# Performance work log

Measured on AMD Instinct MI355X. Metric: run time of the kernel, lower is better.

The kernel has to match this reference:

```python
import math
import jax, jax.numpy as jnp
import numpy as np

B, N, H, K = 8, 1024, 200, 3
EDGE_SIZE = 50

def _layernorm(x, g, b, eps=1e-20):
    mu = jnp.mean(x, -1, keepdims=True)
    var = jnp.mean((x - mu) ** 2, -1, keepdims=True)
    return (x - mu) / jnp.sqrt(var + eps) * g + b

def _bert_layer(x, mask_add, qw, qb, kw, kb, vw, vb, aow, aob, g1, b1, iw, ib, ow, ob, g2, b2):
    # single-head self-attention (num_heads=1 -> head_dim == H), eval mode (dropout = identity)
    q = x @ qw + qb
    k = x @ kw + kb
    v = x @ vw + vb
    scores = jnp.einsum('bnd,bmd->bnm', q, k) / math.sqrt(H) + mask_add  # [B,N,N]
    probs = jax.nn.softmax(scores, -1)
    ctx = jnp.einsum('bnm,bmd->bnd', probs, v)
    attn = _layernorm(ctx @ aow + aob + x, g1, b1)
    inter = jax.nn.gelu(attn @ iw + ib, approximate=False)
    return _layernorm(inter @ ow + ob + attn, g2, b2)

def setup_inputs():
    key = jax.random.key(0)
    ks = jax.random.split(key, 16)
    s = 0.02
    text = jax.random.normal(ks[0], (B, N, H), jnp.float32)
    adj1 = (jax.random.uniform(ks[1], (B, N, N)) < 0.02).astype(jnp.float32)
    adj1 = jnp.maximum(adj1, jnp.eye(N, dtype=jnp.float32))  # self loops
    adj2 = (jax.random.uniform(ks[2], (B, N, N)) < 0.02).astype(jnp.float32)
    edge1 = jax.random.randint(ks[3], (B, N, N), 0, EDGE_SIZE, jnp.int32)
    edge2 = jax.random.randint(ks[4], (B, N, N), 0, EDGE_SIZE, jnp.int32)
    lengths = jax.random.randint(ks[5], (B,), N // 2, N + 1)
    textmask = (jnp.arange(N)[None, :] < lengths[:, None]).astype(jnp.float32)
    def nrm(k, shape):
        return jax.random.normal(k, shape, jnp.float32) * s
    return dict(
        text=text, adj1=adj1, adj2=adj2, edge1=edge1, edge2=edge2, textmask=textmask,
        gcn_w=nrm(ks[6], (H, H)), mut_w=nrm(ks[7], (H, H)),
        qw=nrm(ks[8], (K, H, H)), qb=jnp.zeros((K, H), jnp.float32),
        kw=nrm(ks[9], (K, H, H)), kb=jnp.zeros((K, H), jnp.float32),
        vw=nrm(ks[10], (K, H, H)), vb=jnp.zeros((K, H), jnp.float32),
        aow=nrm(ks[11], (K, H, H)), aob=jnp.zeros((K, H), jnp.float32),
        ln1_g=jnp.ones((K, H), jnp.float32), ln1_b=jnp.zeros((K, H), jnp.float32),
        iw=nrm(ks[12], (K, H, H)), ib=jnp.zeros((K, H), jnp.float32),
        ow=nrm(ks[13], (K, H, H)), ob=jnp.zeros((K, H), jnp.float32),
        ln2_g=jnp.ones((K, H), jnp.float32), ln2_b=jnp.zeros((K, H), jnp.float32))

def reference(text, adj1, adj2, edge1, edge2, textmask, gcn_w, mut_w, qw, qb, kw, kb, vw, vb, aow, aob, ln1_g, ln1_b, iw, ib, ow, ob, ln2_g, ln2_b):
    # edge1/edge2 and edge_vocab are unused by the original forward
    adj = adj1 + adj2
    adj = jnp.where(adj >= 1.0, 1.0, adj)
    mask_add = ((1.0 - textmask) * -10000.0)[:, None, :]           # [B,1,N] key-side mask
    pair = textmask[:, :, None] * textmask[:, None, :]             # [B,N,N]
    pair_add = (1.0 - pair) * -10000.0
    denom = jnp.sum(adj, 2, keepdims=True) + 1e-07                 # [B,N,1]
    outs, output = text, text                                      # in_features == out_features path
    for i in range(K):
        outs = _bert_layer(outs, mask_add, qw[i], qb[i], kw[i], kb[i], vw[i], vb[i],
                           aow[i], aob[i], ln1_g[i], ln1_b[i], iw[i], ib[i], ow[i], ob[i], ln2_g[i], ln2_b[i])
        # GCN propagation: adj-matmul -> degree normalize -> relu -> residual (dropout = identity in eval)
        teout = output @ gcn_w
        output = jax.nn.relu(jnp.einsum('bnm,bmd->bnd', adj, teout) / denom) + output
        # selfalignment: dual masked softmax attention between outs and output
        logit = jnp.einsum('bnd,bmd->bnm', outs @ mut_w, output) + pair_add
        p_row = jax.nn.softmax(logit, -1)
        p_col = jax.nn.softmax(logit, -2)
        new_outs = jnp.einsum('bnm,bmd->bnd', p_row, output) * textmask[:, :, None] + outs
        output = jnp.einsum('bnm,bnd->bmd', p_col, outs) * textmask[:, :, None] + output
        outs = new_outs
    return outs, adj
```

## Files before the change

### kernel.cpp

```cpp
#include <hip/hip_runtime.h>
#include <hip/hip_bf16.h>
#include <math.h>

#define Bd 8
#define Nd 1024
#define Hd 200
#define HP 224
#define BN (Bd*Nd)
#define SZ_BNH ((size_t)BN*Hd)
#define SZ_BNN ((size_t)BN*Nd)
#define SZ_PAD ((size_t)BN*HP)

typedef __hip_bfloat16 bf16;
typedef __attribute__((ext_vector_type(8))) short bf16x8;
typedef __attribute__((ext_vector_type(4))) float f32x4;
typedef __attribute__((ext_vector_type(4))) short s16x4;

__device__ __forceinline__ float bf2f(bf16 v){ return __bfloat162float(v); }
__device__ __forceinline__ bf16 f2bf(float v){ return __float2bfloat16(v); }
__device__ __forceinline__ short bfb(float v){ bf16 h = f2bf(v); return *(short*)&h; }
__device__ __forceinline__ short lowb(float v){
  bf16 h = f2bf(v); bf16 l = f2bf(v - bf2f(h)); return *(short*)&l;
}

#define MFMA16(a,b,c) __builtin_amdgcn_mfma_f32_16x16x32_bf16((a),(b),(c),0,0,0)

__device__ __forceinline__ size_t tidx1024(int row, int k){
  return (size_t)(row>>4)*16384 + (size_t)((k>>5))*512
       + (size_t)(((k>>3)&3))*128 + (size_t)(row&15)*8 + (k&7);
}
__device__ __forceinline__ size_t tidxHP(int row, int k){
  return (size_t)(row>>4)*3584 + (size_t)((k>>5))*512
       + (size_t)(((k>>3)&3))*128 + (size_t)(row&15)*8 + (k&7);
}

__global__ void k_prep_masks(const float* __restrict__ tm, float* __restrict__ maskf,
                             float* __restrict__ maskadd){
  int i = blockIdx.x*256 + threadIdx.x;
  if (i < BN){ float m = tm[i]; maskf[i] = m; maskadd[i] = (1.f - m) * -10000.f; }
}

__global__ void k_prep_adj(const float* __restrict__ a1, const float* __restrict__ a2,
                           float* __restrict__ adj_out, float* __restrict__ denom){
  int r = blockIdx.x;
  const size_t base = (size_t)r * Nd;
  int t = threadIdx.x;
  float s = 0.f;
  for (int m = t; m < Nd; m += 256){
    float a = a1[base+m] + a2[base+m];
    a = a >= 1.f ? 1.f : a;
    adj_out[base+m] = a;
    s += a;
  }
  __shared__ float red[256];
  red[t] = s; __syncthreads();
  for (int st = 128; st > 0; st >>= 1){ if (t < st) red[t] += red[t+st]; __syncthreads(); }
  if (t == 0) denom[r] = red[0] + 1e-07f;
}

__global__ void k_copy2(const float* __restrict__ x, float* __restrict__ o1,
                        float* __restrict__ o2){
  size_t i = (size_t)blockIdx.x*256 + threadIdx.x;
  if (i < SZ_BNH){ float v = x[i]; o1[i] = v; o2[i] = v; }
}

__global__ void c_pad_split(const float* __restrict__ X, bf16* __restrict__ Oh,
                            bf16* __restrict__ Ol){
  size_t o = (size_t)blockIdx.x*256 + threadIdx.x;
  if (o >= SZ_PAD) return;
  int oi = (int)o;
  int panel = oi / 3584;
  int rem   = oi % 3584;
  int kt  = rem >> 9;
  int kg  = (rem >> 7) & 3;
  int r16 = (rem >> 3) & 15;
  int ke  = rem & 7;
  int row = panel*16 + r16;
  int k   = kt*32 + kg*8 + ke;
  float v = (k < Hd) ? X[(size_t)row*Hd + k] : 0.f;
  bf16 h = f2bf(v);
  Oh[o] = h; Ol[o] = f2bf(v - bf2f(h));
}

__global__ void c_padT_split(const float* __restrict__ X, bf16* __restrict__ Oh,
                             bf16* __restrict__ Ol){
  __shared__ float t[32][33];
  int b = blockIdx.z, m0 = blockIdx.x*32, d0 = blockIdx.y*32;
  int tx = threadIdx.x, ty = threadIdx.y;
  for (int i = ty; i < 32; i += 8){
    int d = d0 + tx;
    t[i][tx] = (d < Hd) ? X[((size_t)b*Nd + m0+i)*Hd + d] : 0.f;
  }
  __syncthreads();
  for (int i = ty; i < 32; i += 8){
    int row = d0 + i, kk = m0 + tx;
    size_t idx = (size_t)b*229376 + tidx1024(row, kk);
    float v = t[tx][i];
    bf16 h = f2bf(v);
    Oh[idx] = h; Ol[idx] = f2bf(v - bf2f(h));
  }
}

__global__ void c_w_split_all(const float* __restrict__ g, const float* __restrict__ m,
                              const float* __restrict__ q, const float* __restrict__ k,
                              const float* __restrict__ v, const float* __restrict__ ao,
                              const float* __restrict__ iw, const float* __restrict__ ow,
                              bf16* __restrict__ Oh, bf16* __restrict__ Ol){
  int mi = blockIdx.y;
  const float* W;
  if (mi == 0) W = g;
  else if (mi == 1) W = m;
  else {
    int gi = (mi-2)/3, si = (mi-2)%3;
    const float* bs[6] = {q, k, v, ao, iw, ow};
    W = bs[gi] + (size_t)si*Hd*Hd;
  }
  int o = blockIdx.x*256 + threadIdx.x;
  if (o >= HP*HP) return;
  int panel = o / 3584;
  int rem   = o % 3584;
  int kt  = rem >> 9;
  int kg  = (rem >> 7) & 3;
  int r16 = (rem >> 3) & 15;
  int ke  = rem & 7;
  int n   = panel*16 + r16;
  int kk  = kt*32 + kg*8 + ke;
  float val = (n < Hd && kk < Hd) ? W[kk*Hd + n] : 0.f;
  bf16 h = f2bf(val);
  Oh[(size_t)mi*HP*HP + o] = h; Ol[(size_t)mi*HP*HP + o] = f2bf(val - bf2f(h));
}

__global__ void c_cvt1024_t(const float* __restrict__ X, bf16* __restrict__ O){
  int b = blockIdx.z, kg = blockIdx.x, rg = blockIdx.y;
  int r = threadIdx.x >> 5, kl = threadIdx.x & 31;
  int row = rg*8 + r, k = kg*32 + kl;
  float v = X[(size_t)b*1048576 + (size_t)row*1024 + k];
  O[(size_t)b*1048576 + tidx1024(row, k)] = f2bf(v);
}

__global__ __launch_bounds__(256)
void k_rowsoftmax0(const float* __restrict__ S, bf16* __restrict__ Ph){
  __shared__ float red[256];
  size_t bid = blockIdx.x;
  size_t r = ((bid & 7) << 10) + (bid >> 3);
  int t = threadIdx.x;
  const f32x4 v4 = *(const f32x4*)(S + r*Nd + t*4);
  float mx = fmaxf(fmaxf(v4[0], v4[1]), fmaxf(v4[2], v4[3]));
  red[t] = mx; __syncthreads();
  for (int s = 128; s > 0; s >>= 1){ if (t < s) red[t] = fmaxf(red[t], red[t+s]); __syncthreads(); }
  mx = red[0]; __syncthreads();
  float e0 = __expf(v4[0] - mx), e1 = __expf(v4[1] - mx);
  float e2 = __expf(v4[2] - mx), e3 = __expf(v4[3] - mx);
  red[t] = (e0 + e1) + (e2 + e3); __syncthreads();
  for (int s = 128; s > 0; s >>= 1){ if (t < s) red[t] += red[t+s]; __syncthreads(); }
  float inv = 1.f / red[0];
  size_t obase = ((r >> 10) << 20) + (size_t)(((int)(r & 1023)) >> 4)*16384
               + (size_t)((int)r & 15)*8;
  int i = t*4;
  size_t idx = obase + (size_t)(i>>5)*512 + (size_t)((i>>3)&3)*128 + (i&7);
  s16x4 hv = { bfb(e0*inv), bfb(e1*inv), bfb(e2*inv), bfb(e3*inv) };
  *(s16x4*)(Ph + idx) = hv;
}

__global__ __launch_bounds__(256)
void k_rowsm8(const float* __restrict__ S, bf16* __restrict__ Ph,
              bf16* __restrict__ Pl, const float* __restrict__ cmax,
              const float* __restrict__ csum, bf16* __restrict__ PcH,
              bf16* __restrict__ PcL){
  __shared__ float rows[8][1028];
  int bq = blockIdx.x & 7;
  int rg = blockIdx.x >> 3;
  int n0 = rg*8;
  int t = threadIdx.x;
  int r_loc = t >> 5, j = t & 31;
  size_t r = ((size_t)bq << 10) + n0 + r_loc;
  const float* src = S + r*Nd;
  f32x4 v[8];
  float mx = -3.4e38f;
  #pragma unroll
  for (int kk = 0; kk < 8; kk++){
    v[kk] = *(const f32x4*)(src + kk*128 + j*4);
    *(f32x4*)(&rows[r_loc][kk*128 + j*4]) = v[kk];
    mx = fmaxf(mx, fmaxf(fmaxf(v[kk][0], v[kk][1]), fmaxf(v[kk][2], v[kk][3])));
  }
  #pragma unroll
  for (int off = 16; off >= 1; off >>= 1) mx = fmaxf(mx, __shfl_xor(mx, off));
  float e[8][4];
  float sum = 0.f;
  #pragma unroll
  for (int kk = 0; kk < 8; kk++){
    #pragma unroll
    for (int q = 0; q < 4; q++){ e[kk][q] = __expf(v[kk][q] - mx); }
    sum += (e[kk][0] + e[kk][1]) + (e[kk][2] + e[kk][3]);
  }
  #pragma unroll
  for (int off = 16; off >= 1; off >>= 1) sum += __shfl_xor(sum, off);
  float inv = 1.f / sum;
  size_t obase = ((size_t)bq << 20) + (size_t)((n0 + r_loc) >> 4)*16384
               + (size_t)((n0 + r_loc) & 15)*8;
  #pragma unroll
  for (int kk = 0; kk < 8; kk++){
    int i = kk*128 + j*4;
    size_t idx = obase + (size_t)(i>>5)*512 + (size_t)((i>>3)&3)*128 + (i&7);
    float p0 = e[kk][0]*inv, p1 = e[kk][1]*inv, p2 = e[kk][2]*inv, p3 = e[kk][3]*inv;
    s16x4 hv = { bfb(p0), bfb(p1), bfb(p2), bfb(p3) };
    *(s16x4*)(Ph + idx) = hv;
    s16x4 lv = { lowb(p0), lowb(p1), lowb(p2), lowb(p3) };
    *(s16x4*)(Pl + idx) = lv;
  }
  __syncthreads();
  const f32x4 c4 = *(const f32x4*)(cmax + bq*Nd + t*4);
  const f32x4 s4 = *(const f32x4*)(csum + bq*Nd + t*4);
  size_t nb = (size_t)bq*1048576 + (size_t)(rg>>2)*512 + (size_t)(rg&3)*128;
  #pragma unroll
  for (int mi = 0; mi < 4; mi++){
    int m = t*4 + mi;
    float cm = c4[mi], ci = 1.f / s4[mi];
    bf16x8 hv, lv;
    #pragma unroll
    for (int rr = 0; rr < 8; rr++){
      float p = __expf(rows[rr][m] - cm) * ci;
      bf16 h = f2bf(p);
      hv[rr] = *(short*)&h;
      bf16 l = f2bf(p - bf2f(h));
      lv[rr] = *(short*)&l;
    }
    size_t idx = nb + (size_t)(m>>4)*16384 + (size_t)(m&15)*8;
    *(bf16x8*)(PcH + idx) = hv;
    *(bf16x8*)(PcL + idx) = lv;
  }
}

__global__ void k_colcomb(const float* __restrict__ cpm, const float* __restrict__ cps,
                          float* __restrict__ cmax, float* __restrict__ csum){
  int i = blockIdx.x*256 + threadIdx.x;
  float M = cpm[i], S = cps[i];
  #pragma unroll
  for (int y = 1; y < 8; y++){
    float m2 = cpm[(size_t)y*BN + i], s2 = cps[(size_t)y*BN + i];
    float Mn = fmaxf(M, m2);
    S = S*__expf(M - Mn) + s2*__expf(m2 - Mn);
    M = Mn;
  }
  cmax[i] = M; csum[i] = S;
}

__global__ void k_add_ln(const float* __restrict__ X, const float* __restrict__ R,
                         const float* __restrict__ g, const float* __restrict__ bb,
                         float* __restrict__ Y, bf16* __restrict__ Ph,
                         bf16* __restrict__ Pl){
  int r = blockIdx.x, t = threadIdx.x;
  __shared__ float red[256];
  bool act = t < Hd;
  float v = 0.f;
  if (act) v = X[(size_t)r*Hd + t] + R[(size_t)r*Hd + t];
  red[t] = act ? v : 0.f; __syncthreads();
  for (int s = 128; s > 0; s >>= 1){ if (t < s) red[t] += red[t+s]; __syncthreads(); }
  float mu = red[0] * (1.f/Hd); __syncthreads();
  float d = act ? (v - mu) : 0.f;
  red[t] = d*d; __syncthreads();
  for (int s = 128; s > 0; s >>= 1){ if (t < s) red[t] += red[t+s]; __syncthreads(); }
  float var = red[0] * (1.f/Hd);
  float o = 0.f;
  if (act){
    float rs = 1.f / sqrtf(var + 1e-20f);
    o = (v - mu) * rs * g[t] + bb[t];
    Y[(size_t)r*Hd + t] = o;
  }
  if (Ph && t < HP){
    bf16 h = f2bf(o);
    size_t idx = tidxHP(r, t);
    Ph[idx] = h; Pl[idx] = f2bf(o - bf2f(h));
  }
}

__global__ __launch_bounds__(256)
void k_qkv(const bf16* __restrict__ Ah, const bf16* __restrict__ Al,
           const bf16* __restrict__ Wh0, const bf16* __restrict__ Wl0,
           bf16* __restrict__ QH, bf16* __restrict__ QL,
           bf16* __restrict__ KH, bf16* __restrict__ KL,
           bf16* __restrict__ VH, bf16* __restrict__ VL,
           const float* __restrict__ qb, const float* __restrict__ kb,
           const float* __restrict__ vb)
{
  constexpr int KP = HP;
  constexpr int STEPS = KP/32;
  int slice = blockIdx.z;
  int wave = threadIdx.x >> 6, lane = threadIdx.x & 63;
  int r0 = (blockIdx.y*4 + wave)*16;
  int c0 = blockIdx.x*64;
  int lm = lane & 15, lq = lane >> 4;
  const size_t PST = (size_t)16*KP;
  const size_t aT = (size_t)(r0>>4)*PST + (size_t)lane*8;
  const size_t bT = (size_t)slice*3*HP*HP + (size_t)(c0>>4)*PST + (size_t)lane*8;

  f32x4 acc[4] = {};
  bf16x8 pah[2], pal[2], pbh[2][4], pbl[2][4];
  pah[0] = *(const bf16x8*)(Ah + aT);
  pal[0] = *(const bf16x8*)(Al + aT);
  #pragma unroll
  for (int j = 0; j < 4; j++){
    pbh[0][j] = *(const bf16x8*)(Wh0 + bT + (size_t)j*PST);
    pbl[0][j] = *(const bf16x8*)(Wl0 + bT + (size_t)j*PST);
  }
  #pragma unroll
  for (int ki = 0; ki < STEPS; ki++){
    const int cb = ki & 1, nb = cb ^ 1;
    if (ki + 1 < STEPS){
      const size_t kn = (size_t)(ki+1)*512;
      pah[nb] = *(const bf16x8*)(Ah + aT + kn);
      pal[nb] = *(const bf16x8*)(Al + aT + kn);
      #pragma unroll
      for (int j = 0; j < 4; j++){
        pbh[nb][j] = *(const bf16x8*)(Wh0 + bT + (size_t)j*PST + kn);
        pbl[nb][j] = *(const bf16x8*)(Wl0 + bT + (size_t)j*PST + kn);
      }
    }
    #pragma unroll
    for (int j = 0; j < 4; j++) acc[j] = MFMA16(pah[cb], pbh[cb][j], acc[j]);
    #pragma unroll
    for (int j = 0; j < 4; j++) acc[j] = MFMA16(pah[cb], pbl[cb][j], acc[j]);
    #pragma unroll
    for (int j = 0; j < 4; j++) acc[j] = MFMA16(pal[cb], pbh[cb][j], acc[j]);
  }

  const float* bias = (slice == 0) ? qb : (slice == 1) ? kb : vb;
  if (slice < 2){
    bf16* Oh = (slice == 0) ? QH : KH;
    bf16* Ol = (slice == 0) ? QL : KL;
    #pragma unroll
    for (int j = 0; j < 4; j++){
      int col = c0 + j*16 + lm;
      if (col >= HP) continue;
      #pragma unroll
      for (int r = 0; r < 4; r++){
        int row = r0 + lq*4 + r;
        float o = (col < Hd) ? acc[j][r] + bias[col] : 0.f;
        bf16 h = f2bf(o);
        size_t idx = tidxHP(row, col);
        Oh[idx] = h; Ol[idx] = f2bf(o - bf2f(h));
      }
    }
  } else {
    __shared__ float tl[64][65];
    #pragma unroll
    for (int j = 0; j < 4; j++)
      #pragma unroll
      for (int r = 0; r < 4; r++)
        tl[wave*16 + lq*4 + r][j*16 + lm] = acc[j][r];
    __syncthreads();
    int b2 = (int)((blockIdx.y*64) >> 10);
    int m0 = (int)((blockIdx.y*64) & 1023);
    #pragma unroll
    for (int e = threadIdx.x; e < 4096; e += 256){
      int pan = e >> 10, rem = e & 1023;
      int r16 = (rem >> 3) & 15;
      int d = c0 + pan*16 + r16;
      if (d >= HP) continue;
      int kg = (rem >> 7) & 3;
      int k_loc = (rem >> 9)*32 + kg*8 + (rem & 7);
      float val = 0.f;
      if (d < Hd) val = tl[k_loc][pan*16 + r16] + bias[d];
      bf16 h = f2bf(val);
      size_t idx = (size_t)b2*229376 + (size_t)(d>>4)*16384
                 + (size_t)((m0 + k_loc)>>5)*512 + (size_t)kg*128
                 + (size_t)r16*8 + (rem & 7);
      VH[idx] = h; VL[idx] = f2bf(val - bf2f(h));
    }
  }
}

template<int EPI, int TERMS, int RI, int KP>
__global__ __launch_bounds__(256)
void k_mfma3(const bf16* __restrict__ Ah, const bf16* __restrict__ Al,
             const bf16* __restrict__ Bh, const bf16* __restrict__ Bl,
             float* __restrict__ Y, bf16* __restrict__ Ybh, bf16* __restrict__ Ybl,
             const float* __restrict__ bias, const float* __restrict__ e0,
             const float* __restrict__ e1,
             size_t sAb, size_t sBb, float scale,
             float* __restrict__ cpm, float* __restrict__ cps)
{
  int b = blockIdx.z;
  int wave = threadIdx.x >> 6, lane = threadIdx.x & 63;
  int r0 = (blockIdx.y*4 + wave)*(RI*16);
  int c0 = blockIdx.x*64;
  int lm = lane & 15, lq = lane >> 4;
  const size_t PST = (size_t)16*KP;
  const size_t aT = (size_t)b*sAb + (size_t)(r0>>4)*PST + (size_t)lane*8;
  const size_t bT = (size_t)b*sBb + (size_t)(c0>>4)*PST + (size_t)lane*8;
  constexpr int STEPS = KP/32;

  f32x4 acc[RI][4] = {};
  bf16x8 pah[2][RI], pal[2][RI], pbh[2][4], pbl[2][4];
  {
    #pragma unroll
    for (int i = 0; i < RI; i++) pah[0][i] = *(const bf16x8*)(Ah + aT + (size_t)i*PST);
    #pragma unroll
    for (int j = 0; j < 4; j++){
      pbh[0][j] = *(const bf16x8*)(Bh + bT + (size_t)j*PST);
      pbl[0][j] = *(const bf16x8*)(Bl + bT + (size_t)j*PST);
    }
    if (TERMS >= 3){
      #pragma unroll
      for (int i = 0; i < RI; i++) pal[0][i] = *(const bf16x8*)(Al + aT + (size_t)i*PST);
    }
  }

  #pragma unroll
  for (int ki = 0; ki < STEPS; ki++){
    const int cb = ki & 1, nb = cb ^ 1;
    if (ki + 1 < STEPS){
      const size_t kn = (size_t)(ki+1)*512;
      #pragma unroll
      for (int i = 0; i < RI; i++) pah[nb][i] = *(const bf16x8*)(Ah + aT + (size_t)i*PST + kn);
      #pragma unroll
      for (int j = 0; j < 4; j++){
        pbh[nb][j] = *(const bf16x8*)(Bh + bT + (size_t)j*PST + kn);
        pbl[nb][j] = *(const bf16x8*)(Bl + bT + (size_t)j*PST + kn);
      }
      if (TERMS >= 3){
        #pragma unroll
        for (int i = 0; i < RI; i++) pal[nb][i] = *(const bf16x8*)(Al + aT + (size_t)i*PST + kn);
      }
    }
    #pragma unroll
    for (int i = 0; i < RI; i++)
      #pragma unroll
      for (int j = 0; j < 4; j++) acc[i][j] = MFMA16(pah[cb][i], pbh[cb][j], acc[i][j]);
    #pragma unroll
    for (int i = 0; i < RI; i++)
      #pragma unroll
      for (int j = 0; j < 4; j++) acc[i][j] = MFMA16(pah[cb][i], pbl[cb][j], acc[i][j]);
    if (TERMS >= 3){
      #pragma unroll
      for (int i = 0; i < RI; i++)
        #pragma unroll
        for (int j = 0; j < 4; j++) acc[i][j] = MFMA16(pal[cb][i], pbh[cb][j], acc[i][j]);
    }
  }

  if constexpr (EPI == 9){
    __shared__ float tl[64][65];
    #pragma unroll
    for (int j = 0; j < 4; j++)
      #pragma unroll
      for (int r = 0; r < 4; r++)
        tl[wave*16 + lq*4 + r][j*16 + lm] = acc[0][j][r];
    __syncthreads();
    int b2 = (int)((blockIdx.y*64) >> 10);
    int m0 = (int)((blockIdx.y*64) & 1023);
    #pragma unroll
    for (int e = threadIdx.x; e < 4096; e += 256){
      int pan = e >> 10, rem = e & 1023;
      int r16 = (rem >> 3) & 15;
      int d = c0 + pan*16 + r16;
      if (d >= HP) continue;
      int kg = (rem >> 7) & 3;
      int k_loc = (rem >> 9)*32 + kg*8 + (rem & 7);
      float val = 0.f;
      if (d < Hd) val = tl[k_loc][pan*16 + r16] + (bias ? bias[d] : 0.f);
      bf16 h = f2bf(val);
      size_t idx = (size_t)b2*229376 + (size_t)(d>>4)*16384
                 + (size_t)((m0 + k_loc)>>5)*512 + (size_t)kg*128
                 + (size_t)r16*8 + (rem & 7);
      Ybh[idx] = h; Ybl[idx] = f2bf(val - bf2f(h));
    }
  } else if constexpr (EPI == 4){
    float er[RI][4];
    #pragma unroll
    for (int i = 0; i < RI; i++)
      #pragma unroll
      for (int r = 0; r < 4; r++)
        er[i][r] = e1[b*Nd + r0 + i*16 + lq*4 + r];
    float cm[4], cs[4];
    #pragma unroll
    for (int j = 0; j < 4; j++){
      int col = c0 + j*16 + lm;
      float e1c = e1[b*Nd + col];
      float wv[RI][4];
      float mloc = -3.4e38f;
      #pragma unroll
      for (int i = 0; i < RI; i++){
        #pragma unroll
        for (int r = 0; r < 4; r++){
          int row = r0 + i*16 + lq*4 + r;
          float w = acc[i][j][r] + (1.f - er[i][r]*e1c)*(-10000.f);
          Y[((size_t)b*Nd + row)*Nd + col] = w;
          wv[i][r] = w;
          mloc = fmaxf(mloc, w);
        }
      }
      float sloc = 0.f;
      #pragma unroll
      for (int i = 0; i < RI; i++)
        #pragma unroll
        for (int r = 0; r < 4; r++) sloc += __expf(wv[i][r] - mloc);
      cm[j] = mloc; cs[j] = sloc;
    }
    #pragma unroll
    for (int j = 0; j < 4; j++){
      float m = cm[j], s = cs[j];
      #pragma unroll
      for (int off = 16; off <= 32; off <<= 1){
        float m2 = __shfl_xor(m, off), s2 = __shfl_xor(s, off);
        float M = fmaxf(m, m2);
        s = s*__expf(m - M) + s2*__expf(m2 - M);
        m = M;
      }
      cm[j] = m; cs[j] = s;
    }
    __shared__ float pmx[4][4][16], psm[4][4][16];
    if (lq == 0){
      #pragma unroll
      for (int j = 0; j < 4; j++){ pmx[wave][j][lm] = cm[j]; psm[wave][j][lm] = cs[j]; }
    }
    __syncthreads();
    if (threadIdx.x < 64){
      int t = threadIdx.x;
      int jj = t >> 4, cc = t & 15;
      float M = pmx[0][jj][cc], S = psm[0][jj][cc];
      #pragma unroll
      for (int w = 1; w < 4; w++){
        float m2 = pmx[w][jj][cc], s2 = psm[w][jj][cc];
        float Mn = fmaxf(M, m2);
        S = S*__expf(M - Mn) + s2*__expf(m2 - Mn);
        M = Mn;
      }
      size_t pi = (size_t)blockIdx.y*BN + (size_t)b*Nd + c0 + t;
      cpm[pi] = M; cps[pi] = S;
    }
  } else {
    #pragma unroll
    for (int i = 0; i < RI; i++){
      #pragma unroll
      for (int j = 0; j < 4; j++){
        int col = c0 + j*16 + lm;
        int rbase = r0 + i*16 + lq*4;
        #pragma unroll
        for (int r = 0; r < 4; r++){
          int row = rbase + r;
          size_t rowg = (size_t)b*Nd + row;
          float v = acc[i][j][r];
          if (EPI == 0){
            if (col < Hd){
              v += bias ? bias[col] : 0.f;
              Y[rowg*Hd + col] = v;
            }
          } else if (EPI == 2){
            if (col < HP){
              float o = (col < Hd) ? v + (bias ? bias[col] : 0.f) : 0.f;
              bf16 h = f2bf(o);
              size_t idx = tidxHP((int)rowg, col);
              Ybh[idx] = h;
              Ybl[idx] = f2bf(o - bf2f(h));
            }
          } else if (EPI == 3){
            Y[rowg*Nd + col] = v*scale + e0[b*Nd + col];
          } else if (EPI == 10){
            if (col < HP){
              float o = 0.f;
              if (col < Hd){
                float vv = v + (bias ? bias[col] : 0.f);
                o = 0.5f*vv*(1.f + erff(vv*0.7071067811865476f));
              }
              bf16 h = f2bf(o);
              size_t idx = tidxHP((int)rowg, col);
              Ybh[idx] = h;
              Ybl[idx] = f2bf(o - bf2f(h));
            }
          }
        }
      }
    }
  }
}

template<int EPI, int TERMS, int KP>
__global__ __launch_bounds__(256)
void k_mfma3sk(const bf16* __restrict__ Ah, const bf16* __restrict__ Al,
               const bf16* __restrict__ Bh, const bf16* __restrict__ Bl,
               float* __restrict__ Y, bf16* __restrict__ Ybh, bf16* __restrict__ Ybl,
               const float* __restrict__ e0, const float* __restrict__ e1,
               const float* __restrict__ R,
               size_t sAb, size_t sBb,
               bf16* __restrict__ TbH, bf16* __restrict__ TbL)
{
  __shared__ float red[4][64][33];
  int b = blockIdx.z;
  int wave = threadIdx.x >> 6, lane = threadIdx.x & 63;
  int r0 = blockIdx.x*32;
  int c0 = blockIdx.y*64;
  int lm = lane & 15, lq = lane >> 4;
  const size_t aT = (size_t)b*sAb + (size_t)(r0>>4)*((size_t)16*KP) + (size_t)lane*8;
  const size_t bT = (size_t)b*sBb + (size_t)(c0>>4)*((size_t)16*KP) + (size_t)lane*8;
  const int kt0 = wave*(KP>>7);
  constexpr int STEPS = KP/128;

  f32x4 acc[2][4] = {};
  bf16x8 pah[2][2], pal[2][2], pbh[2][4], pbl[2][4];
  {
    const size_t ko = (size_t)kt0*512;
    #pragma unroll
    for (int i = 0; i < 2; i++) pah[0][i] = *(const bf16x8*)(Ah + aT + (size_t)(i*16)*KP + ko);
    #pragma unroll
    for (int j = 0; j < 4; j++){
      pbh[0][j] = *(const bf16x8*)(Bh + bT + (size_t)(j*16)*KP + ko);
      pbl[0][j] = *(const bf16x8*)(Bl + bT + (size_t)(j*16)*KP + ko);
    }
    if (TERMS >= 3){
      #pragma unroll
      for (int i = 0; i < 2; i++) pal[0][i] = *(const bf16x8*)(Al + aT + (size_t)(i*16)*KP + ko);
    }
  }

  #pragma unroll
  for (int ki = 0; ki < STEPS; ki++){
    const int cb = ki & 1, nb = cb ^ 1;
    if (ki + 1 < STEPS){
      const size_t kn = (size_t)(kt0 + ki + 1)*512;
      #pragma unroll
      for (int i = 0; i < 2; i++) pah[nb][i] = *(const bf16x8*)(Ah + aT + (size_t)(i*16)*KP + kn);
      #pragma unroll
      for (int j = 0; j < 4; j++){
        pbh[nb][j] = *(const bf16x8*)(Bh + bT + (size_t)(j*16)*KP + kn);
        pbl[nb][j] = *(const bf16x8*)(Bl + bT + (size_t)(j*16)*KP + kn);
      }
      if (TERMS >= 3){
        #pragma unroll
        for (int i = 0; i < 2; i++) pal[nb][i] = *(const bf16x8*)(Al + aT + (size_t)(i*16)*KP + kn);
      }
    }
    #pragma unroll
    for (int i = 0; i < 2; i++)
      #pragma unroll
      for (int j = 0; j < 4; j++) acc[i][j] = MFMA16(pah[cb][i], pbh[cb][j], acc[i][j]);
    #pragma unroll
    for (int i = 0; i < 2; i++)
      #pragma unroll
      for (int j = 0; j < 4; j++) acc[i][j] = MFMA16(pah[cb][i], pbl[cb][j], acc[i][j]);
    if (TERMS >= 3){
      #pragma unroll
      for (int i = 0; i < 2; i++)
        #pragma unroll
        for (int j = 0; j < 4; j++) acc[i][j] = MFMA16(pal[cb][i], pbh[cb][j], acc[i][j]);
    }
  }

  #pragma unroll
  for (int i = 0; i < 2; i++)
    #pragma unroll
    for (int j = 0; j < 4; j++)
      #pragma unroll
      for (int r = 0; r < 4; r++)
        red[wave][lane][i*16 + j*4 + r] = acc[i][j][r];
  __syncthreads();

  int iw = wave >> 1, j0 = (wave & 1)*2;
  #pragma unroll
  for (int jj = 0; jj < 2; jj++){
    int j = j0 + jj;
    int col = c0 + j*16 + lm;
    #pragma unroll
    for (int r = 0; r < 4; r++){
      int f = iw*16 + j*4 + r;
      float v = red[0][lane][f] + red[1][lane][f] + red[2][lane][f] + red[3][lane][f];
      int row = r0 + iw*16 + lq*4 + r;
      size_t rowg = (size_t)b*Nd + row;
      if (col < HP){
        float nv = 0.f;
        if (EPI == 8){
          nv = (col < Hd) ? v : 0.f;
        } else if (EPI == 5){
          if (col < Hd){
            float u = v / e0[b*Nd+row]; u = u > 0.f ? u : 0.f;
            nv = Y[rowg*Hd + col] + u;
            Y[rowg*Hd + col] = nv;
          }
        } else if (EPI == 6){
          if (col < Hd){
            nv = v*e1[b*Nd+row] + R[rowg*Hd+col];
            Y[rowg*Hd + col] = nv;
          }
        } else if (EPI == 7){
          if (col < Hd){
            nv = v*e1[b*Nd+row] + Y[rowg*Hd+col];
            Y[rowg*Hd + col] = nv;
          }
        }
        bf16 h = f2bf(nv);
        bf16 lo = f2bf(nv - bf2f(h));
        size_t idx = tidxHP((int)rowg, col);
        Ybh[idx] = h; Ybl[idx] = lo;
        if (TbH != nullptr){
          size_t idx2 = (size_t)b*((size_t)HP*Nd) + tidx1024(col, row);
          TbH[idx2] = h; TbL[idx2] = lo;
        }
      }
    }
  }
}

static inline char* carve(char*& p, size_t bytes){
  char* r = p;
  p += (bytes + 511) & ~(size_t)511;
  return r;
}

extern "C" void kernel_launch(void* const* d_in, const int* in_sizes, int n_in,
                              void* d_out, int out_size, void* d_ws, size_t ws_size,
                              hipStream_t stream){
  (void)in_sizes; (void)n_in; (void)out_size; (void)ws_size;
  const float* text     = (const float*)d_in[0];
  const float* adj1     = (const float*)d_in[1];
  const float* adj2     = (const float*)d_in[2];
  const float* textmask = (const float*)d_in[5];
  const float* gcn_w    = (const float*)d_in[6];
  const float* mut_w    = (const float*)d_in[7];
  const float* qw = (const float*)d_in[8],  *qb = (const float*)d_in[9];
  const float* kw = (const float*)d_in[10], *kb = (const float*)d_in[11];
  const float* vw = (const float*)d_in[12], *vb = (const float*)d_in[13];
  const float* aow= (const float*)d_in[14], *aob= (const float*)d_in[15];
  const float* g1 = (const float*)d_in[16], *b1 = (const float*)d_in[17];
  const float* iw = (const float*)d_in[18], *ib = (const float*)d_in[19];
  const float* ow = (const float*)d_in[20], *ob = (const float*)d_in[21];
  const float* g2 = (const float*)d_in[22], *b2 = (const float*)d_in[23];

  float* out_outs = (float*)d_out;
  float* out_adj  = out_outs + SZ_BNH;

  char* p = (char*)d_ws;
  float* cur  = (float*)carve(p, SZ_BNH*4);
  float* sc1  = (float*)carve(p, SZ_BNH*4);
  float* fo   = (float*)carve(p, SZ_BNH*4);
  float* S    = (float*)carve(p, SZ_BNN*4);
  bf16*  Rb   = (bf16*)carve(p, SZ_BNN*2*2);
  bf16*  Rc   = (bf16*)carve(p, SZ_BNN*2*2);
  bf16*  T1   = (bf16*)carve(p, SZ_PAD*2);
  bf16*  T2   = (bf16*)carve(p, SZ_PAD*2);
  bf16*  T3   = (bf16*)carve(p, SZ_PAD*2);
  bf16*  T4   = (bf16*)carve(p, SZ_PAD*2);
  bf16*  T5   = (bf16*)carve(p, SZ_PAD*2);
  bf16*  T6   = (bf16*)carve(p, SZ_PAD*2);
  bf16*  TA1  = (bf16*)carve(p, SZ_PAD*2);
  bf16*  TA2  = (bf16*)carve(p, SZ_PAD*2);
  bf16*  TF1  = (bf16*)carve(p, SZ_PAD*2);
  bf16*  TF2  = (bf16*)carve(p, SZ_PAD*2);
  bf16*  TT1  = (bf16*)carve(p, SZ_PAD*2);
  bf16*  TT2  = (bf16*)carve(p, SZ_PAD*2);
  bf16*  ADJB = (bf16*)carve(p, SZ_BNN*2);
  bf16*  Wh_all = (bf16*)carve(p, (size_t)21*HP*HP*2);
  bf16*  Wl_all = (bf16*)carve(p, (size_t)21*HP*HP*2);
  float* cpm     = (float*)carve(p, (size_t)8*BN*4);
  float* cps     = (float*)carve(p, (size_t)8*BN*4);
  float* denom   = (float*)carve(p, BN*4);
  float* maskf   = (float*)carve(p, BN*4);
  float* maskadd = (float*)carve(p, BN*4);
  float* cmaxv   = (float*)carve(p, BN*4);
  float* csumv   = (float*)carve(p, BN*4);

  float* sc2 = out_outs;
  bf16* attnP = Rb;
  bf16* Ph    = Rb;
  bf16* Pl    = Rb + SZ_BNN;
  bf16* PcH   = Rc;
  bf16* PcL   = Rc + SZ_BNN;

  const size_t sNT = (size_t)Nd*HP;
  const size_t sT  = (size_t)HP*Nd;
  const size_t sNN = (size_t)Nd*Nd;

  #define W_GCN 0
  #define W_MUT 1
  #define W_Q(i) (2 + (i))
  #define W_K(i) (5 + (i))
  #define W_V(i) (8 + (i))
  #define W_AO(i) (11 + (i))
  #define W_IW(i) (14 + (i))
  #define W_OW(i) (17 + (i))
  #define WH(s) (Wh_all + (size_t)(s)*HP*HP)
  #define WL(s) (Wl_all + (size_t)(s)*HP*HP)

  dim3 blk256(256);
  dim3 gPad((unsigned)((SZ_PAD+255)/256));
  dim3 gPadT(32, 7, Bd), bT(32, 8);
  dim3 gWall((HP*HP+255)/256, 20);
  dim3 gCvt(32, 128, Bd);
  dim3 gBNH((unsigned)((SZ_BNH+255)/256));
  dim3 gSm(4, 128, 1);
  dim3 gQKV(4, 128, 3);
  dim3 gNT(16, 8, Bd);
  dim3 gSK(32, 4, Bd);
  const float inv_sqrt_h = 0.07071067811865475f;
  const size_t Z = 0;
  float* FN = nullptr;
  bf16*  BN_ = nullptr;

  k_prep_masks<<<(BN+255)/256, blk256, 0, stream>>>(textmask, maskf, maskadd);
  k_prep_adj<<<BN, blk256, 0, stream>>>(adj1, adj2, out_adj, denom);
  k_copy2<<<gBNH, blk256, 0, stream>>>(text, cur, fo);
  c_w_split_all<<<gWall, blk256, 0, stream>>>(gcn_w, mut_w, qw, kw, vw, aow, iw, ow,
                                              Wh_all, Wl_all);
  c_pad_split<<<gPad, blk256, 0, stream>>>(text, TA1, TA2);
  c_pad_split<<<gPad, blk256, 0, stream>>>(text, TF1, TF2);
  c_cvt1024_t<<<gCvt, blk256, 0, stream>>>(out_adj, ADJB);

  for (int i = 0; i < 3; i++){
    const float *qbi = qb + i*Hd;
    const float *kbi = kb + i*Hd;
    const float *vbi = vb + i*Hd;
    const float *aobi= aob+ i*Hd;
    const float *g1i = g1 + i*Hd,    *b1i = b1 + i*Hd;
    const float *ibi = ib + i*Hd;
    const float *obi = ob + i*Hd;
    const float *g2i = g2 + i*Hd,    *b2i = b2 + i*Hd;

    k_qkv<<<gQKV, blk256, 0, stream>>>(TA1,TA2, WH(W_Q(i)),WL(W_Q(i)),
              T3,T4, T5,T6, T1,T2, qbi,kbi,vbi);
    k_mfma3<3,3,2,HP><<<gNT, blk256, 0, stream>>>(T3,T4,T5,T6, S,BN_,BN_,
              nullptr, maskadd,nullptr, sNT,sNT, inv_sqrt_h, FN,FN);
    k_rowsoftmax0<<<BN, blk256, 0, stream>>>(S, attnP);
    k_mfma3sk<8,2,Nd><<<gSK, blk256, 0, stream>>>(attnP,BN_,T1,T2,
              FN,T3,T4, FN,FN,FN, sNN,sT, BN_,BN_);
    k_mfma3<0,3,1,HP><<<gSm, blk256, 0, stream>>>(T3,T4,WH(W_AO(i)),WL(W_AO(i)),
              sc1,BN_,BN_, aobi, FN,FN, Z,Z, 0.f, FN,FN);
    k_add_ln<<<BN, blk256, 0, stream>>>(sc1, cur, g1i, b1i, sc2, T1, T2);
    k_mfma3<10,3,1,HP><<<gSm, blk256, 0, stream>>>(T1,T2,WH(W_IW(i)),WL(W_IW(i)),
              FN,T3,T4, ibi, FN,FN, Z,Z, 0.f, FN,FN);
    k_mfma3<0,3,1,HP><<<gSm, blk256, 0, stream>>>(T3,T4,WH(W_OW(i)),WL(W_OW(i)),
              cur,BN_,BN_, obi, FN,FN, Z,Z, 0.f, FN,FN);
    k_add_ln<<<BN, blk256, 0, stream>>>(cur, sc2, g2i, b2i, cur, TA1, TA2);

    k_mfma3<9,3,1,HP><<<gSm, blk256, 0, stream>>>(TF1,TF2,WH(W_GCN),WL(W_GCN),
              FN,T1,T2, nullptr, FN,FN, Z,Z, 0.f, FN,FN);
    k_mfma3sk<5,2,Nd><<<gSK, blk256, 0, stream>>>(ADJB,BN_,T1,T2,
              fo,TF1,TF2, denom,FN,FN, sNN,sT, TT1,TT2);

    k_mfma3<2,3,1,HP><<<gSm, blk256, 0, stream>>>(TA1,TA2,WH(W_MUT),WL(W_MUT),
              FN,T5,T6, nullptr, FN,FN, Z,Z, 0.f, FN,FN);
    k_mfma3<4,3,2,HP><<<gNT, blk256, 0, stream>>>(T5,T6,TF1,TF2, S,BN_,BN_,
              nullptr, nullptr,maskf, sNT,sNT, 0.f, cpm,cps);
    k_colcomb<<<BN/256, blk256, 0, stream>>>(cpm, cps, cmaxv, csumv);
    k_rowsm8<<<BN/8, blk256, 0, stream>>>(S, Ph, Pl, cmaxv, csumv, PcH, PcL);
    c_padT_split<<<gPadT, bT, 0, stream>>>(cur, T3, T4);
    k_mfma3sk<6,3,Nd><<<gSK, blk256, 0, stream>>>(Ph,Pl,TT1,TT2,
              (i==2)?out_outs:sc1, TA1,TA2, FN,maskf,cur, sNN,sT, BN_,BN_);
    k_mfma3sk<7,3,Nd><<<gSK, blk256, 0, stream>>>(PcH,PcL,T3,T4,
              fo,TF1,TF2, FN,maskf,FN, sNN,sT, BN_,BN_);

    float* t = cur; cur = sc1; sc1 = t;
  }
}
```

Measured before the change: 1.106 ms.

## Replace split-K P@V GEMM with per-wave row tiles without LDS reduction

The N-by-H GEMMs with K=1024 previously split K across four waves per block and reduced the partial sums through shared memory. Now each wave owns a distinct 16-row tile and walks the full K range itself, which removes the LDS reduction and the barrier. The grid shrinks from 32x4x8 to 16x4x8 blocks while each wave runs a longer serial K loop. Each B tile load is no longer reused across two row tiles, so B-operand traffic per MFMA rises.

```diff
diff --git a/kernel.cpp b/kernel.cpp
--- a/kernel.cpp
+++ b/kernel.cpp
@@ -575,9 +575,9 @@
   }
 }
 
-template<int EPI, int TERMS, int KP>
+template<int EPI, int TERMS>
 __global__ __launch_bounds__(256)
-void k_mfma3sk(const bf16* __restrict__ Ah, const bf16* __restrict__ Al,
+void k_mfma3nk(const bf16* __restrict__ Ah, const bf16* __restrict__ Al,
                const bf16* __restrict__ Bh, const bf16* __restrict__ Bl,
                float* __restrict__ Y, bf16* __restrict__ Ybh, bf16* __restrict__ Ybl,
                const float* __restrict__ e0, const float* __restrict__ e1,
@@ -585,87 +585,56 @@
                size_t sAb, size_t sBb,
                bf16* __restrict__ TbH, bf16* __restrict__ TbL)
 {
-  __shared__ float red[4][64][33];
+  constexpr int KP = Nd;
+  constexpr int STEPS = KP/32;
   int b = blockIdx.z;
   int wave = threadIdx.x >> 6, lane = threadIdx.x & 63;
-  int r0 = blockIdx.x*32;
+  int r0 = (blockIdx.x*4 + wave)*16;
   int c0 = blockIdx.y*64;
   int lm = lane & 15, lq = lane >> 4;
   const size_t aT = (size_t)b*sAb + (size_t)(r0>>4)*((size_t)16*KP) + (size_t)lane*8;
   const size_t bT = (size_t)b*sBb + (size_t)(c0>>4)*((size_t)16*KP) + (size_t)lane*8;
-  const int kt0 = wave*(KP>>7);
-  constexpr int STEPS = KP/128;
-
-  f32x4 acc[2][4] = {};
-  bf16x8 pah[2][2], pal[2][2], pbh[2][4], pbl[2][4];
-  {
-    const size_t ko = (size_t)kt0*512;
-    #pragma unroll
-    for (int i = 0; i < 2; i++) pah[0][i] = *(const bf16x8*)(Ah + aT + (size_t)(i*16)*KP + ko);
-    #pragma unroll
-    for (int j = 0; j < 4; j++){
-      pbh[0][j] = *(const bf16x8*)(Bh + bT + (size_t)(j*16)*KP + ko);
-      pbl[0][j] = *(const bf16x8*)(Bl + bT + (size_t)(j*16)*KP + ko);
-    }
-    if (TERMS >= 3){
-      #pragma unroll
-      for (int i = 0; i < 2; i++) pal[0][i] = *(const bf16x8*)(Al + aT + (size_t)(i*16)*KP + ko);
-    }
-  }
-
+
+  f32x4 acc[4] = {};
+  bf16x8 pah[2], pal[2], pbh[2][4], pbl[2][4];
+  pah[0] = *(const bf16x8*)(Ah + aT);
+  if (TERMS >= 3) pal[0] = *(const bf16x8*)(Al + aT);
+  #pragma unroll
+  for (int j = 0; j < 4; j++){
+    pbh[0][j] = *(const bf16x8*)(Bh + bT + (size_t)(j*16)*KP);
+    pbl[0][j] = *(const bf16x8*)(Bl + bT + (size_t)(j*16)*KP);
+  }
   #pragma unroll
   for (int ki = 0; ki < STEPS; ki++){
     const int cb = ki & 1, nb = cb ^ 1;
     if (ki + 1 < STEPS){
-      const size_t kn = (size_t)(kt0 + ki + 1)*512;
-      #pragma unroll
-      for (int i = 0; i < 2; i++) pah[nb][i] = *(const bf16x8*)(Ah + aT + (size_t)(i*16)*KP + kn);
+      const size_t kn = (size_t)(ki+1)*512;
+      pah[nb] = *(const bf16x8*)(Ah + aT + kn);
+      if (TERMS >= 3) pal[nb] = *(const bf16x8*)(Al + aT + kn);
       #pragma unroll
       for (int j = 0; j < 4; j++){
         pbh[nb][j] = *(const bf16x8*)(Bh + bT + (size_t)(j*16)*KP + kn);
         pbl[nb][j] = *(const bf16x8*)(Bl + bT + (size_t)(j*16)*KP + kn);
       }
-      if (TERMS >= 3){
-        #pragma unroll
-        for (int i = 0; i < 2; i++) pal[nb][i] = *(const bf16x8*)(Al + aT + (size_t)(i*16)*KP + kn);
-      }
-    }
-    #pragma unroll
-    for (int i = 0; i < 2; i++)
-      #pragma unroll
-      for (int j = 0; j < 4; j++) acc[i][j] = MFMA16(pah[cb][i], pbh[cb][j], acc[i][j]);
-    #pragma unroll
-    for (int i = 0; i < 2; i++)
-      #pragma unroll
-      for (int j = 0; j < 4; j++) acc[i][j] = MFMA16(pah[cb][i], pbl[cb][j], acc[i][j]);
+    }
+    #pragma unroll
+    for (int j = 0; j < 4; j++) acc[j] = MFMA16(pah[cb], pbh[cb][j], acc[j]);
+    #pragma unroll
+    for (int j = 0; j < 4; j++) acc[j] = MFMA16(pah[cb], pbl[cb][j], acc[j]);
     if (TERMS >= 3){
       #pragma unroll
-      for (int i = 0; i < 2; i++)
-        #pragma unroll
-        for (int j = 0; j < 4; j++) acc[i][j] = MFMA16(pal[cb][i], pbh[cb][j], acc[i][j]);
-    }
-  }
-
-  #pragma unroll
-  for (int i = 0; i < 2; i++)
-    #pragma unroll
-    for (int j = 0; j < 4; j++)
-      #pragma unroll
-      for (int r = 0; r < 4; r++)
-        red[wave][lane][i*16 + j*4 + r] = acc[i][j][r];
-  __syncthreads();
-
-  int iw = wave >> 1, j0 = (wave & 1)*2;
-  #pragma unroll
-  for (int jj = 0; jj < 2; jj++){
-    int j = j0 + jj;
+      for (int j = 0; j < 4; j++) acc[j] = MFMA16(pal[cb], pbh[cb][j], acc[j]);
+    }
+  }
+
+  #pragma unroll
+  for (int j = 0; j < 4; j++){
     int col = c0 + j*16 + lm;
     #pragma unroll
     for (int r = 0; r < 4; r++){
-      int f = iw*16 + j*4 + r;
-      float v = red[0][lane][f] + red[1][lane][f] + red[2][lane][f] + red[3][lane][f];
-      int row = r0 + iw*16 + lq*4 + r;
+      int row = r0 + lq*4 + r;
       size_t rowg = (size_t)b*Nd + row;
+      float v = acc[j][r];
       if (col < HP){
         float nv = 0.f;
         if (EPI == 8){
@@ -789,7 +758,7 @@
   dim3 gSm(4, 128, 1);
   dim3 gQKV(4, 128, 3);
   dim3 gNT(16, 8, Bd);
-  dim3 gSK(32, 4, Bd);
+  dim3 gNK(16, 4, Bd);
   const float inv_sqrt_h = 0.07071067811865475f;
   const size_t Z = 0;
   float* FN = nullptr;
@@ -819,7 +788,7 @@
     k_mfma3<3,3,2,HP><<<gNT, blk256, 0, stream>>>(T3,T4,T5,T6, S,BN_,BN_,
               nullptr, maskadd,nullptr, sNT,sNT, inv_sqrt_h, FN,FN);
     k_rowsoftmax0<<<BN, blk256, 0, stream>>>(S, attnP);
-    k_mfma3sk<8,2,Nd><<<gSK, blk256, 0, stream>>>(attnP,BN_,T1,T2,
+    k_mfma3nk<8,2><<<gNK, blk256, 0, stream>>>(attnP,BN_,T1,T2,
               FN,T3,T4, FN,FN,FN, sNN,sT, BN_,BN_);
     k_mfma3<0,3,1,HP><<<gSm, blk256, 0, stream>>>(T3,T4,WH(W_AO(i)),WL(W_AO(i)),
               sc1,BN_,BN_, aobi, FN,FN, Z,Z, 0.f, FN,FN);
@@ -832,7 +801,7 @@
 
     k_mfma3<9,3,1,HP><<<gSm, blk256, 0, stream>>>(TF1,TF2,WH(W_GCN),WL(W_GCN),
               FN,T1,T2, nullptr, FN,FN, Z,Z, 0.f, FN,FN);
-    k_mfma3sk<5,2,Nd><<<gSK, blk256, 0, stream>>>(ADJB,BN_,T1,T2,
+    k_mfma3nk<5,2><<<gNK, blk256, 0, stream>>>(ADJB,BN_,T1,T2,
               fo,TF1,TF2, denom,FN,FN, sNN,sT, TT1,TT2);
 
     k_mfma3<2,3,1,HP><<<gSm, blk256, 0, stream>>>(TA1,TA2,WH(W_MUT),WL(W_MUT),
@@ -842,9 +811,9 @@
     k_colcomb<<<BN/256, blk256, 0, stream>>>(cpm, cps, cmaxv, csumv);
     k_rowsm8<<<BN/8, blk256, 0, stream>>>(S, Ph, Pl, cmaxv, csumv, PcH, PcL);
     c_padT_split<<<gPadT, bT, 0, stream>>>(cur, T3, T4);
-    k_mfma3sk<6,3,Nd><<<gSK, blk256, 0, stream>>>(Ph,Pl,TT1,TT2,
+    k_mfma3nk<6,3><<<gNK, blk256, 0, stream>>>(Ph,Pl,TT1,TT2,
               (i==2)?out_outs:sc1, TA1,TA2, FN,maskf,cur, sNN,sT, BN_,BN_);
-    k_mfma3sk<7,3,Nd><<<gSK, blk256, 0, stream>>>(PcH,PcL,T3,T4,
+    k_mfma3nk<7,3><<<gNK, blk256, 0, stream>>>(PcH,PcL,T3,T4,
               fo,TF1,TF2, FN,maskf,FN, sNN,sT, BN_,BN_);
 
     float* t = cur; cur = sc1; sc1 = t;
```

Result: slower. 1.270 ms (+14.8%).
